# Optimization experiments

Measured on AMD Instinct MI355X. Metric: run time of the kernel, lower is better.

Reference implementation:

```python
import jax, jax.numpy as jnp
import numpy as np

FEATURE_SIZE = 10 * 64 * 64  # 40960
HIDDEN1 = 512
HIDDEN2 = 256
BATCH = 4096


def setup_inputs() -> dict:
    key = jax.random.key(0)
    ks = jax.random.split(key, 8)
    # Sparse binary-ish features emulated as dense uniform (math is identical).
    white_features = jax.random.uniform(ks[0], (BATCH, FEATURE_SIZE), dtype=jnp.float32)
    black_features = jax.random.uniform(ks[1], (BATCH, FEATURE_SIZE), dtype=jnp.float32)
    s_ft = 1.0 / np.sqrt(FEATURE_SIZE)
    s_fc1 = 1.0 / np.sqrt(HIDDEN1 * 2)
    s_fc2 = 1.0 / np.sqrt(HIDDEN2)
    ft_w = jax.random.uniform(ks[2], (HIDDEN1, FEATURE_SIZE), minval=-s_ft, maxval=s_ft, dtype=jnp.float32)
    ft_b = jax.random.uniform(ks[3], (HIDDEN1,), minval=-s_ft, maxval=s_ft, dtype=jnp.float32)
    fc1_w = jax.random.uniform(ks[4], (HIDDEN2, HIDDEN1 * 2), minval=-s_fc1, maxval=s_fc1, dtype=jnp.float32)
    fc1_b = jax.random.uniform(ks[5], (HIDDEN2,), minval=-s_fc1, maxval=s_fc1, dtype=jnp.float32)
    fc2_w = jax.random.uniform(ks[6], (1, HIDDEN2), minval=-s_fc2, maxval=s_fc2, dtype=jnp.float32)
    fc2_b = jax.random.uniform(ks[7], (1,), minval=-s_fc2, maxval=s_fc2, dtype=jnp.float32)
    return dict(white_features=white_features, black_features=black_features,
                ft_w=ft_w, ft_b=ft_b, fc1_w=fc1_w, fc1_b=fc1_b, fc2_w=fc2_w, fc2_b=fc2_b)


def reference(white_features, black_features, ft_w, ft_b, fc1_w, fc1_b, fc2_w, fc2_b):
    # Feature transform per perspective, clamped to [0, 1]
    white_ft = jnp.clip(white_features @ ft_w.T + ft_b, 0.0, 1.0)  # [B, H1]
    black_ft = jnp.clip(black_features @ ft_w.T + ft_b, 0.0, 1.0)  # [B, H1]
    combined = jnp.concatenate([white_ft, black_ft], axis=1)       # [B, 2*H1]
    x = jax.nn.relu(combined @ fc1_w.T + fc1_b)                    # [B, H2]
    x = x @ fc2_w.T + fc2_b                                        # [B, 1]
    return x.squeeze(-1)
```

## Files before the change

kernel.cpp:

```cpp
#include <hip/hip_runtime.h>
#include <stdint.h>

#define BATCH 4096
#define FEAT  40960
#define H1    512
#define KS    4
#define KCHUNK (FEAT / KS)
#define NSTEPS (KCHUNK / 32)
#define NTILES (FEAT / 32)
#define WTILE  32768
#define BUFSTRIDE 36864
#define ALDS 32768

typedef float f32x4 __attribute__((ext_vector_type(4)));
typedef short s16x8 __attribute__((ext_vector_type(8)));
typedef unsigned int u32x2 __attribute__((ext_vector_type(2)));
typedef unsigned int u32x4 __attribute__((ext_vector_type(4)));

__device__ __forceinline__ unsigned bfpack2(float lo, float hi) {
  unsigned a = __float_as_uint(lo);
  unsigned b = __float_as_uint(hi);
  a += 0x7FFFu + ((a >> 16) & 1u);
  b += 0x7FFFu + ((b >> 16) & 1u);
  return (a >> 16) | (b & 0xFFFF0000u);
}

__device__ __forceinline__ int lds_swz(int r, int cb) {
  return (r << 6) + (cb ^ (((r >> 1) & 3) << 4));
}

__device__ __forceinline__ void glds16(const void* g, void* l) {
  __builtin_amdgcn_global_load_lds(
      (const __attribute__((address_space(1))) unsigned*)g,
      (__attribute__((address_space(3))) unsigned*)l, 16, 0, 0);
}

__global__ __launch_bounds__(512)
void wcvt_kernel(const float* __restrict__ ftw, char* __restrict__ wbf) {
  const int bid = blockIdx.x;
  const int T = bid >> 2, rq = bid & 3;
  const int tid = threadIdx.x;
  const int r = rq * 128 + (tid >> 2), kq = tid & 3;
  const float* src = ftw + (size_t)r * FEAT + T * 32 + kq * 8;
  f32x4 v0 = *(const f32x4*)src;
  f32x4 v1 = *(const f32x4*)(src + 4);
  u32x4 o;
  o.x = bfpack2(v0.x, v0.y); o.y = bfpack2(v0.z, v0.w);
  o.z = bfpack2(v1.x, v1.y); o.w = bfpack2(v1.z, v1.w);
  *(u32x4*)(wbf + (size_t)T * WTILE + lds_swz(r, kq * 16)) = o;
}

__global__ __launch_bounds__(512, 4)
void ft_gemm_kernel(const float* __restrict__ whiteF,
                    const float* __restrict__ blackF,
                    const char* __restrict__ wbf,
                    float* __restrict__ Ppart) {
  __shared__ char smem[2 * BUFSTRIDE];

  const int tid = threadIdx.x, bid = blockIdx.x;
  const int wgid = (bid & 7) * 64 + (bid >> 3);
  const int ks = wgid >> 7;
  const int p  = (wgid >> 6) & 1;
  const int mt = wgid & 63;

  const float* Ag =
      (p == 0 ? whiteF : blackF) + (size_t)(mt * 64) * FEAT + ks * KCHUNK;

  const int a_row = tid >> 3, a_kq = tid & 7;
  const float* aptr = Ag + (size_t)a_row * FEAT + a_kq * 4;
  const int awoff = ALDS + lds_swz(a_row, a_kq * 8);

  const int lane = tid & 63, wave = tid >> 6;
  const char* wsrc = wbf + (size_t)ks * NSTEPS * WTILE + wave * 4096 + lane * 16;
  const int wdst = wave * 4096;

  const int wn = wave;
  const int lrow = lane & 15, lkb = (lane >> 4) * 16;
  int a_off[4], b_off[4];
#pragma unroll
  for (int m = 0; m < 4; ++m) a_off[m] = ALDS + lds_swz(m * 16 + lrow, lkb);
#pragma unroll
  for (int n = 0; n < 4; ++n) b_off[n] = lds_swz(wn * 64 + n * 16 + lrow, lkb);

  f32x4 acc[4][4];
#pragma unroll
  for (int m = 0; m < 4; ++m)
#pragma unroll
    for (int n = 0; n < 4; ++n) acc[m][n] = (f32x4){0.f, 0.f, 0.f, 0.f};

  f32x4 raA[2];

#pragma unroll
  for (int c = 0; c < 4; ++c) glds16(wsrc + c * 1024, smem + wdst + c * 1024);
  raA[0] = *(const f32x4*)aptr;

#define GSTEP(B, LAST, t)                                                     \
  {                                                                           \
    if (!(LAST)) raA[(B) ^ 1] = *(const f32x4*)(aptr + (size_t)((t) + 1) * 32); \
    u32x2 av;                                                                 \
    av.x = bfpack2(raA[B].x, raA[B].y);                                       \
    av.y = bfpack2(raA[B].z, raA[B].w);                                       \
    *(u32x2*)(smem + (B) * BUFSTRIDE + awoff) = av;                           \
    __builtin_amdgcn_sched_barrier(0);                                        \
    if (LAST) { asm volatile("s_waitcnt vmcnt(0) lgkmcnt(0)" ::: "memory"); } \
    else      { asm volatile("s_waitcnt vmcnt(1) lgkmcnt(0)" ::: "memory"); } \
    __builtin_amdgcn_sched_barrier(0);                                        \
    __builtin_amdgcn_s_barrier();                                             \
    __builtin_amdgcn_sched_barrier(0);                                        \
    const char* base = smem + (B) * BUFSTRIDE;                                \
    s16x8 af[4];                                                              \
    _Pragma("unroll") for (int m = 0; m < 4; ++m)                             \
        af[m] = *(const s16x8*)(base + a_off[m]);                             \
    if (!(LAST)) {                                                            \
      const char* wsp = wsrc + (size_t)((t) + 1) * WTILE;                     \
      char* wdp = smem + ((B) ^ 1) * BUFSTRIDE + wdst;                        \
      _Pragma("unroll") for (int c = 0; c < 4; ++c)                           \
          glds16(wsp + c * 1024, wdp + c * 1024);                             \
    }                                                                         \
    _Pragma("unroll") for (int n = 0; n < 4; ++n) {                           \
      s16x8 bfn = *(const s16x8*)(base + b_off[n]);                           \
      _Pragma("unroll") for (int m = 0; m < 4; ++m)                           \
          acc[m][n] = __builtin_amdgcn_mfma_f32_16x16x32_bf16(                \
              af[m], bfn, acc[m][n], 0, 0, 0);                                \
    }                                                                         \
  }

  for (int tt = 0; tt < NSTEPS - 2; tt += 2) {
    GSTEP(0, false, tt);
    GSTEP(1, false, tt + 1);
  }
  GSTEP(0, false, NSTEPS - 2);
  GSTEP(1, true, NSTEPS - 1);
#undef GSTEP

  float* Pp = Ppart + ((size_t)(ks * 2 + p) * BATCH + mt * 64) * H1;
  const int r0 = (lane >> 4) * 4;
  const int c0 = wn * 64 + lrow;
#pragma unroll
  for (int m = 0; m < 4; ++m)
#pragma unroll
    for (int n = 0; n < 4; ++n) {
      float* dst = Pp + (size_t)(r0 + m * 16) * H1 + c0 + n * 16;
#pragma unroll
      for (int j = 0; j < 4; ++j) dst[(size_t)j * H1] = acc[m][n][j];
    }
}

__global__ __launch_bounds__(256)
void ft_reduce_kernel(const float* __restrict__ Ppart,
                      const float* __restrict__ ftb,
                      unsigned short* __restrict__ comb) {
  const size_t gid = (size_t)blockIdx.x * 256 + threadIdx.x;
  const int    pp  = (int)(gid / (BATCH * H1 / 4));
  const size_t rem = gid % (BATCH * H1 / 4);
  const int    row = (int)(rem / (H1 / 4));
  const int    n4  = (int)(rem % (H1 / 4)) * 4;

  f32x4 s = (f32x4){0.f, 0.f, 0.f, 0.f};
#pragma unroll
  for (int ks = 0; ks < KS; ++ks)
    s += *(const f32x4*)(Ppart + ((size_t)(ks * 2 + pp) * BATCH + row) * H1 + n4);
  const f32x4 bv = *(const f32x4*)(ftb + n4);
  s += bv;
  s.x = fminf(fmaxf(s.x, 0.f), 1.f);
  s.y = fminf(fmaxf(s.y, 0.f), 1.f);
  s.z = fminf(fmaxf(s.z, 0.f), 1.f);
  s.w = fminf(fmaxf(s.w, 0.f), 1.f);

  u32x2 o;
  o.x = bfpack2(s.x, s.y);
  o.y = bfpack2(s.z, s.w);
  *(u32x2*)(comb + (size_t)row * 1024 + pp * H1 + n4) = o;
}

__global__ __launch_bounds__(256)
void fc_kernel(const unsigned short* __restrict__ comb,
               const float* __restrict__ w1, const float* __restrict__ b1,
               const float* __restrict__ w2, const float* __restrict__ b2,
               float* __restrict__ out) {
  __shared__ char smem[40960];
  __shared__ float rowsum[64];

  const int tid = threadIdx.x;
  const int bm  = blockIdx.x;
  if (tid < 64) rowsum[tid] = 0.f;

  const int a_row = tid >> 2, a_kq = tid & 3;
  const unsigned short* aptr = comb + (size_t)(bm * 64 + a_row) * 1024 + a_kq * 8;
  const float* wptr = w1 + (size_t)a_row * 1024 + a_kq * 8;

  u32x4 raA;
  f32x4 rw0[4], rw1[4];
  auto issue = [&](int t) {
    raA = *(const u32x4*)(aptr + t * 32);
    const float* wp = wptr + t * 32;
#pragma unroll
    for (int s = 0; s < 4; ++s) {
      rw0[s] = *(const f32x4*)(wp + (size_t)s * 64 * 1024);
      rw1[s] = *(const f32x4*)(wp + (size_t)s * 64 * 1024 + 4);
    }
  };

  const int aoff_w = lds_swz(a_row, a_kq * 16);
  int woff_w[4];
#pragma unroll
  for (int s = 0; s < 4; ++s)
    woff_w[s] = 4096 + lds_swz(s * 64 + a_row, a_kq * 16);

  auto cvtwrite = [&](int b) {
    char* base = smem + b * 20480;
    *(u32x4*)(base + aoff_w) = raA;
#pragma unroll
    for (int s = 0; s < 4; ++s) {
      u32x4 wv;
      wv.x = bfpack2(rw0[s].x, rw0[s].y); wv.y = bfpack2(rw0[s].z, rw0[s].w);
      wv.z = bfpack2(rw1[s].x, rw1[s].y); wv.w = bfpack2(rw1[s].z, rw1[s].w);
      *(u32x4*)(base + woff_w[s]) = wv;
    }
  };

  const int lane = tid & 63, wn = tid >> 6;
  const int lrow = lane & 15, lkb = (lane >> 4) * 16;
  int a_off[4], b_off[4];
#pragma unroll
  for (int m = 0; m < 4; ++m) a_off[m] = lds_swz(m * 16 + lrow, lkb);
#pragma unroll
  for (int n = 0; n < 4; ++n) b_off[n] = 4096 + lds_swz(wn * 64 + n * 16 + lrow, lkb);

  f32x4 acc[4][4];
#pragma unroll
  for (int m = 0; m < 4; ++m)
#pragma unroll
    for (int n = 0; n < 4; ++n) acc[m][n] = (f32x4){0.f, 0.f, 0.f, 0.f};

  issue(0);
  for (int t = 0; t < 32; ++t) {
    const int b = t & 1;
    cvtwrite(b);
    if (t + 1 < 32) issue(t + 1);
    asm volatile("s_waitcnt lgkmcnt(0)" ::: "memory");
    __builtin_amdgcn_sched_barrier(0);
    __builtin_amdgcn_s_barrier();
    __builtin_amdgcn_sched_barrier(0);
    char* base = smem + b * 20480;
    s16x8 af[4];
#pragma unroll
    for (int m = 0; m < 4; ++m) af[m] = *(const s16x8*)(base + a_off[m]);
#pragma unroll
    for (int n = 0; n < 4; ++n) {
      s16x8 bfn = *(const s16x8*)(base + b_off[n]);
#pragma unroll
      for (int m = 0; m < 4; ++m)
        acc[m][n] = __builtin_amdgcn_mfma_f32_16x16x32_bf16(af[m], bfn, acc[m][n], 0, 0, 0);
    }
  }

  float b1v[4], w2v[4];
#pragma unroll
  for (int n = 0; n < 4; ++n) {
    const int col = wn * 64 + n * 16 + lrow;
    b1v[n] = b1[col];
    w2v[n] = w2[col];
  }
#pragma unroll
  for (int m = 0; m < 4; ++m)
#pragma unroll
    for (int j = 0; j < 4; ++j) {
      float v = 0.f;
#pragma unroll
      for (int n = 0; n < 4; ++n) {
        float x = acc[m][n][j] + b1v[n];
        x = fmaxf(x, 0.f);
        v += x * w2v[n];
      }
#pragma unroll
      for (int d = 1; d < 16; d <<= 1) v += __shfl_xor(v, d, 64);
      if ((lane & 15) == 0)
        atomicAdd(&rowsum[m * 16 + (lane >> 4) * 4 + j], v);
    }
  __syncthreads();
  if (tid < 64) {
    out[bm * 64 + tid] = rowsum[tid] + b2[0];
  }
}

extern "C" void kernel_launch(void* const* d_in, const int* in_sizes, int n_in,
                              void* d_out, int out_size, void* d_ws, size_t ws_size,
                              hipStream_t stream) {
  const float* whiteF = (const float*)d_in[0];
  const float* blackF = (const float*)d_in[1];
  const float* ftw    = (const float*)d_in[2];
  const float* ftb    = (const float*)d_in[3];
  const float* w1     = (const float*)d_in[4];
  const float* b1     = (const float*)d_in[5];
  const float* w2     = (const float*)d_in[6];
  const float* b2     = (const float*)d_in[7];

  char* wbf = (char*)d_ws;
  const size_t wbf_bytes   = (size_t)NTILES * WTILE;
  const size_t ppart_bytes = (size_t)KS * 2 * BATCH * H1 * sizeof(float);
  float* Ppart = (float*)((char*)d_ws + wbf_bytes);
  unsigned short* comb = (unsigned short*)((char*)d_ws + wbf_bytes + ppart_bytes);
  float* outp = (float*)d_out;

  hipLaunchKernelGGL(wcvt_kernel, dim3(NTILES * 4), dim3(512), 0, stream, ftw, wbf);
  hipLaunchKernelGGL(ft_gemm_kernel, dim3(512), dim3(512), 0, stream,
                     whiteF, blackF, wbf, Ppart);
  hipLaunchKernelGGL(ft_reduce_kernel, dim3((2 * BATCH * H1 / 4) / 256), dim3(256),
                     0, stream, Ppart, ftb, comb);
  hipLaunchKernelGGL(fc_kernel, dim3(BATCH / 64), dim3(256), 0, stream,
                     comb, w1, b1, w2, b2, outp);
}
```

Baseline: 548.8 us.

## Load A fragments directly into registers and drop the workgroup barrier

The activation tile no longer goes through LDS. Each wave now loads its own MFMA A fragments straight from global memory, converts them with the hardware v_cvt_pk_bf16_f32 instruction, and prefetches the next step's fragments into registers. Because each wave only reads the weight region it copies into LDS itself, the per-step s_barrier is removed and the LDS footprint shrinks to two 32 KB weight buffers. The trade-off is that the A tile is read eight times per workgroup, once per wave, from global/cache, which adds cache traffic and register pressure.

```diff
diff --git a/kernel.cpp b/kernel.cpp
--- a/kernel.cpp
+++ b/kernel.cpp
@@ -9,8 +9,6 @@
 #define NSTEPS (KCHUNK / 32)
 #define NTILES (FEAT / 32)
 #define WTILE  32768
-#define BUFSTRIDE 36864
-#define ALDS 32768
 
 typedef float f32x4 __attribute__((ext_vector_type(4)));
 typedef short s16x8 __attribute__((ext_vector_type(8)));
@@ -23,6 +21,12 @@
   a += 0x7FFFu + ((a >> 16) & 1u);
   b += 0x7FFFu + ((b >> 16) & 1u);
   return (a >> 16) | (b & 0xFFFF0000u);
+}
+
+__device__ __forceinline__ unsigned cvtpk(float lo, float hi) {
+  unsigned r;
+  asm("v_cvt_pk_bf16_f32 %0, %1, %2" : "=v"(r) : "v"(lo), "v"(hi));
+  return r;
 }
 
 __device__ __forceinline__ int lds_swz(int r, int cb) {
@@ -55,7 +59,7 @@
                     const float* __restrict__ blackF,
                     const char* __restrict__ wbf,
                     float* __restrict__ Ppart) {
-  __shared__ char smem[2 * BUFSTRIDE];
+  __shared__ char smem[65536];
 
   const int tid = threadIdx.x, bid = blockIdx.x;
   const int wgid = (bid & 7) * 64 + (bid >> 3);
@@ -66,19 +70,19 @@
   const float* Ag =
       (p == 0 ? whiteF : blackF) + (size_t)(mt * 64) * FEAT + ks * KCHUNK;
 
-  const int a_row = tid >> 3, a_kq = tid & 7;
-  const float* aptr = Ag + (size_t)a_row * FEAT + a_kq * 4;
-  const int awoff = ALDS + lds_swz(a_row, a_kq * 8);
-
   const int lane = tid & 63, wave = tid >> 6;
+  const int lrow = lane & 15, lkb = (lane >> 4) * 16;
+
+  const float* am[4];
+#pragma unroll
+  for (int m = 0; m < 4; ++m)
+    am[m] = Ag + (size_t)(m * 16 + lrow) * FEAT + (lane >> 4) * 8;
+
   const char* wsrc = wbf + (size_t)ks * NSTEPS * WTILE + wave * 4096 + lane * 16;
   const int wdst = wave * 4096;
 
   const int wn = wave;
-  const int lrow = lane & 15, lkb = (lane >> 4) * 16;
-  int a_off[4], b_off[4];
-#pragma unroll
-  for (int m = 0; m < 4; ++m) a_off[m] = ALDS + lds_swz(m * 16 + lrow, lkb);
+  int b_off[4];
 #pragma unroll
   for (int n = 0; n < 4; ++n) b_off[n] = lds_swz(wn * 64 + n * 16 + lrow, lkb);
 
@@ -88,35 +92,47 @@
 #pragma unroll
     for (int n = 0; n < 4; ++n) acc[m][n] = (f32x4){0.f, 0.f, 0.f, 0.f};
 
-  f32x4 raA[2];
+  f32x4 raf[4][2];
 
 #pragma unroll
   for (int c = 0; c < 4; ++c) glds16(wsrc + c * 1024, smem + wdst + c * 1024);
-  raA[0] = *(const f32x4*)aptr;
+#pragma unroll
+  for (int m = 0; m < 4; ++m) {
+    raf[m][0] = *(const f32x4*)am[m];
+    raf[m][1] = *(const f32x4*)(am[m] + 4);
+  }
 
 #define GSTEP(B, LAST, t)                                                     \
   {                                                                           \
-    if (!(LAST)) raA[(B) ^ 1] = *(const f32x4*)(aptr + (size_t)((t) + 1) * 32); \
-    u32x2 av;                                                                 \
-    av.x = bfpack2(raA[B].x, raA[B].y);                                       \
-    av.y = bfpack2(raA[B].z, raA[B].w);                                       \
-    *(u32x2*)(smem + (B) * BUFSTRIDE + awoff) = av;                           \
+    asm volatile("s_waitcnt lgkmcnt(0)" ::: "memory");  \
     __builtin_amdgcn_sched_barrier(0);                                        \
-    if (LAST) { asm volatile("s_waitcnt vmcnt(0) lgkmcnt(0)" ::: "memory"); } \
-    else      { asm volatile("s_waitcnt vmcnt(1) lgkmcnt(0)" ::: "memory"); } \
-    __builtin_amdgcn_sched_barrier(0);                                        \
-    __builtin_amdgcn_s_barrier();                                             \
-    __builtin_amdgcn_sched_barrier(0);                                        \
-    const char* base = smem + (B) * BUFSTRIDE;                                \
-    s16x8 af[4];                                                              \
-    _Pragma("unroll") for (int m = 0; m < 4; ++m)                             \
-        af[m] = *(const s16x8*)(base + a_off[m]);                             \
     if (!(LAST)) {                                                            \
       const char* wsp = wsrc + (size_t)((t) + 1) * WTILE;                     \
-      char* wdp = smem + ((B) ^ 1) * BUFSTRIDE + wdst;                        \
+      char* wdp = smem + ((B) ^ 1) * 32768 + wdst;                            \
       _Pragma("unroll") for (int c = 0; c < 4; ++c)                           \
           glds16(wsp + c * 1024, wdp + c * 1024);                             \
     }                                                                         \
+    __builtin_amdgcn_sched_barrier(0);                                        \
+    if (LAST) { asm volatile("s_waitcnt vmcnt(0)" ::: "memory"); }            \
+    else      { asm volatile("s_waitcnt vmcnt(4)" ::: "memory"); }            \
+    __builtin_amdgcn_sched_barrier(0);                                        \
+    s16x8 af[4];                                                              \
+    _Pragma("unroll") for (int m = 0; m < 4; ++m) {                           \
+      u32x4 cv;                                                               \
+      cv.x = cvtpk(raf[m][0].x, raf[m][0].y);                                 \
+      cv.y = cvtpk(raf[m][0].z, raf[m][0].w);                                 \
+      cv.z = cvtpk(raf[m][1].x, raf[m][1].y);                                 \
+      cv.w = cvtpk(raf[m][1].z, raf[m][1].w);                                 \
+      af[m] = __builtin_bit_cast(s16x8, cv);                                  \
+    }                                                                         \
+    if (!(LAST)) {                                                            \
+      _Pragma("unroll") for (int m = 0; m < 4; ++m) {                         \
+        const float* ap = am[m] + (size_t)((t) + 1) * 32;                     \
+        raf[m][0] = *(const f32x4*)ap;                                        \
+        raf[m][1] = *(const f32x4*)(ap + 4);                                  \
+      }                                                                       \
+    }                                                                         \
+    const char* base = smem + (B) * 32768;                                    \
     _Pragma("unroll") for (int n = 0; n < 4; ++n) {                           \
       s16x8 bfn = *(const s16x8*)(base + b_off[n]);                           \
       _Pragma("unroll") for (int m = 0; m < 4; ++m)                           \
```

Result: slower. 1.462 ms (+166.5%).

## Load B fragments directly from pre-swizzled global into registers, skip LDS staging

Applied to the files above, without the earlier changes.

The weight-conversion kernel now writes bf16 weights in MFMA fragment order, so each lane's B operand is one contiguous 16-byte chunk. The GEMM loads B fragments straight from global memory into double-buffered registers instead of staging them through LDS. LDS is cut to a small double buffer for the A tile. This removes the B-tile LDS traffic and frees shared memory, at the cost of more VGPRs and exposing global-load latency that the old pipeline hid behind barriers.

```diff
diff --git a/kernel.cpp b/kernel.cpp
--- a/kernel.cpp
+++ b/kernel.cpp
@@ -9,8 +9,6 @@
 #define NSTEPS (KCHUNK / 32)
 #define NTILES (FEAT / 32)
 #define WTILE  32768
-#define BUFSTRIDE 36864
-#define ALDS 32768
 
 typedef float f32x4 __attribute__((ext_vector_type(4)));
 typedef short s16x8 __attribute__((ext_vector_type(8)));
@@ -29,25 +27,25 @@
   return (r << 6) + (cb ^ (((r >> 1) & 3) << 4));
 }
 
-__device__ __forceinline__ void glds16(const void* g, void* l) {
-  __builtin_amdgcn_global_load_lds(
-      (const __attribute__((address_space(1))) unsigned*)g,
-      (__attribute__((address_space(3))) unsigned*)l, 16, 0, 0);
-}
-
 __global__ __launch_bounds__(512)
 void wcvt_kernel(const float* __restrict__ ftw, char* __restrict__ wbf) {
-  const int bid = blockIdx.x;
-  const int T = bid >> 2, rq = bid & 3;
+  const int T = blockIdx.x;
   const int tid = threadIdx.x;
-  const int r = rq * 128 + (tid >> 2), kq = tid & 3;
-  const float* src = ftw + (size_t)r * FEAT + T * 32 + kq * 8;
-  f32x4 v0 = *(const f32x4*)src;
-  f32x4 v1 = *(const f32x4*)(src + 4);
-  u32x4 o;
-  o.x = bfpack2(v0.x, v0.y); o.y = bfpack2(v0.z, v0.w);
-  o.z = bfpack2(v1.x, v1.y); o.w = bfpack2(v1.z, v1.w);
-  *(u32x4*)(wbf + (size_t)T * WTILE + lds_swz(r, kq * 16)) = o;
+  const int c  = tid & 7;
+  const int r0 = tid >> 3;
+#pragma unroll
+  for (int pass = 0; pass < 8; ++pass) {
+    const int r = pass * 64 + r0;
+    const float* src = ftw + (size_t)r * FEAT + T * 32 + c * 4;
+    f32x4 v = *(const f32x4*)src;
+    u32x2 o;
+    o.x = bfpack2(v.x, v.y);
+    o.y = bfpack2(v.z, v.w);
+    const int nb = r >> 6, f = (r >> 4) & 3, lr = r & 15;
+    const int l = (c >> 1) * 16 + lr;
+    *(u32x2*)(wbf + (size_t)T * WTILE + ((nb * 4 + f) << 10) + l * 16 +
+              (c & 1) * 8) = o;
+  }
 }
 
 __global__ __launch_bounds__(512, 4)
@@ -55,7 +53,7 @@
                     const float* __restrict__ blackF,
                     const char* __restrict__ wbf,
                     float* __restrict__ Ppart) {
-  __shared__ char smem[2 * BUFSTRIDE];
+  __shared__ char smem[8192];
 
   const int tid = threadIdx.x, bid = blockIdx.x;
   const int wgid = (bid & 7) * 64 + (bid >> 3);
@@ -66,21 +64,19 @@
   const float* Ag =
       (p == 0 ? whiteF : blackF) + (size_t)(mt * 64) * FEAT + ks * KCHUNK;
 
-  const int a_row = tid >> 3, a_kq = tid & 7;
-  const float* aptr = Ag + (size_t)a_row * FEAT + a_kq * 4;
-  const int awoff = ALDS + lds_swz(a_row, a_kq * 8);
+  const int a_row = tid >> 3, a_kc = tid & 7;
+  const float* aptr = Ag + (size_t)a_row * FEAT + a_kc * 4;
+  const int awoff = lds_swz(a_row, a_kc * 8);
 
   const int lane = tid & 63, wave = tid >> 6;
-  const char* wsrc = wbf + (size_t)ks * NSTEPS * WTILE + wave * 4096 + lane * 16;
-  const int wdst = wave * 4096;
-
-  const int wn = wave;
   const int lrow = lane & 15, lkb = (lane >> 4) * 16;
-  int a_off[4], b_off[4];
-#pragma unroll
-  for (int m = 0; m < 4; ++m) a_off[m] = ALDS + lds_swz(m * 16 + lrow, lkb);
-#pragma unroll
-  for (int n = 0; n < 4; ++n) b_off[n] = lds_swz(wn * 64 + n * 16 + lrow, lkb);
+
+  const char* wsrc =
+      wbf + (size_t)ks * NSTEPS * WTILE + (wave << 12) + lane * 16;
+
+  int a_off[4];
+#pragma unroll
+  for (int m = 0; m < 4; ++m) a_off[m] = lds_swz(m * 16 + lrow, lkb);
 
   f32x4 acc[4][4];
 #pragma unroll
@@ -88,37 +84,38 @@
 #pragma unroll
     for (int n = 0; n < 4; ++n) acc[m][n] = (f32x4){0.f, 0.f, 0.f, 0.f};
 
-  f32x4 raA[2];
-
-#pragma unroll
-  for (int c = 0; c < 4; ++c) glds16(wsrc + c * 1024, smem + wdst + c * 1024);
-  raA[0] = *(const f32x4*)aptr;
+  f32x4 raA;
+  u32x4 rb[2][4];
+
+  raA = *(const f32x4*)aptr;
+#pragma unroll
+  for (int n = 0; n < 4; ++n)
+    rb[0][n] = *(const u32x4*)(wsrc + (n << 10));
 
 #define GSTEP(B, LAST, t)                                                     \
   {                                                                           \
-    if (!(LAST)) raA[(B) ^ 1] = *(const f32x4*)(aptr + (size_t)((t) + 1) * 32); \
+                    \
     u32x2 av;                                                                 \
-    av.x = bfpack2(raA[B].x, raA[B].y);                                       \
-    av.y = bfpack2(raA[B].z, raA[B].w);                                       \
-    *(u32x2*)(smem + (B) * BUFSTRIDE + awoff) = av;                           \
-    __builtin_amdgcn_sched_barrier(0);                                        \
-    if (LAST) { asm volatile("s_waitcnt vmcnt(0) lgkmcnt(0)" ::: "memory"); } \
-    else      { asm volatile("s_waitcnt vmcnt(1) lgkmcnt(0)" ::: "memory"); } \
+    av.x = bfpack2(raA.x, raA.y);                                             \
+    av.y = bfpack2(raA.z, raA.w);                                             \
+    *(u32x2*)(smem + (B) * 4096 + awoff) = av;                                \
+    if (!(LAST)) {    \
+      raA = *(const f32x4*)(aptr + (size_t)((t) + 1) * 32);                   \
+                                             \
+      const char* wsp = wsrc + (size_t)((t) + 1) * WTILE;                     \
+      _Pragma("unroll") for (int n = 0; n < 4; ++n)                           \
+          rb[(B) ^ 1][n] = *(const u32x4*)(wsp + (n << 10));                  \
+    }                                                                         \
+    asm volatile("s_waitcnt lgkmcnt(0)" ::: "memory");   \
     __builtin_amdgcn_sched_barrier(0);                                        \
     __builtin_amdgcn_s_barrier();                                             \
     __builtin_amdgcn_sched_barrier(0);                                        \
-    const char* base = smem + (B) * BUFSTRIDE;                                \
+    const char* base = smem + (B) * 4096;                                     \
     s16x8 af[4];                                                              \
     _Pragma("unroll") for (int m = 0; m < 4; ++m)                             \
         af[m] = *(const s16x8*)(base + a_off[m]);                             \
-    if (!(LAST)) {                                                            \
-      const char* wsp = wsrc + (size_t)((t) + 1) * WTILE;                     \
-      char* wdp = smem + ((B) ^ 1) * BUFSTRIDE + wdst;                        \
-      _Pragma("unroll") for (int c = 0; c < 4; ++c)                           \
-          glds16(wsp + c * 1024, wdp + c * 1024);                             \
-    }                                                                         \
     _Pragma("unroll") for (int n = 0; n < 4; ++n) {                           \
-      s16x8 bfn = *(const s16x8*)(base + b_off[n]);                           \
+      s16x8 bfn = __builtin_bit_cast(s16x8, rb[B][n]);                        \
       _Pragma("unroll") for (int m = 0; m < 4; ++m)                           \
           acc[m][n] = __builtin_amdgcn_mfma_f32_16x16x32_bf16(                \
               af[m], bfn, acc[m][n], 0, 0, 0);                                \
@@ -135,7 +132,7 @@
 
   float* Pp = Ppart + ((size_t)(ks * 2 + p) * BATCH + mt * 64) * H1;
   const int r0 = (lane >> 4) * 4;
-  const int c0 = wn * 64 + lrow;
+  const int c0 = wave * 64 + lrow;
 #pragma unroll
   for (int m = 0; m < 4; ++m)
 #pragma unroll
@@ -303,7 +300,7 @@
   unsigned short* comb = (unsigned short*)((char*)d_ws + wbf_bytes + ppart_bytes);
   float* outp = (float*)d_out;
 
-  hipLaunchKernelGGL(wcvt_kernel, dim3(NTILES * 4), dim3(512), 0, stream, ftw, wbf);
+  hipLaunchKernelGGL(wcvt_kernel, dim3(NTILES), dim3(512), 0, stream, ftw, wbf);
   hipLaunchKernelGGL(ft_gemm_kernel, dim3(512), dim3(512), 0, stream,
                      whiteF, blackF, wbf, Ppart);
   hipLaunchKernelGGL(ft_reduce_kernel, dim3((2 * BATCH * H1 / 4) / 256), dim3(256),
```

Result: no change. 553.6 us (+0.9%).

## Enlarge FT GEMM tile to 256x256 with K=64 steps and phased MFMA pipeline

Applied to the files above, without the earlier changes.

Restructures the feature-transform GEMM so each workgroup computes a 256-row by 256-column tile with 64-wide K steps. Each workgroup now covers half of H1 instead of all of it, and the weight image is repacked into an MFMA-fragment-friendly layout. The main loop is split into barrier-separated phases with setprio around MFMA bursts, and activations are prefetched two steps ahead in registers. The aim is more data reuse per LDS byte and less A-matrix global traffic per FLOP, at the cost of 128KB LDS, higher register pressure, lower occupancy and only 256 workgroups.

```diff
diff --git a/kernel.cpp b/kernel.cpp
--- a/kernel.cpp
+++ b/kernel.cpp
@@ -6,11 +6,10 @@
 #define H1    512
 #define KS    4
 #define KCHUNK (FEAT / KS)
-#define NSTEPS (KCHUNK / 32)
-#define NTILES (FEAT / 32)
-#define WTILE  32768
-#define BUFSTRIDE 36864
-#define ALDS 32768
+#define NT    (KCHUNK / 64)
+#define NT64  (FEAT / 64)
+#define WIMG  65536
+#define ABOFF 65536
 
 typedef float f32x4 __attribute__((ext_vector_type(4)));
 typedef short s16x8 __attribute__((ext_vector_type(8)));
@@ -35,109 +34,201 @@
       (__attribute__((address_space(3))) unsigned*)l, 16, 0, 0);
 }
 
+#define PHASE_BAR()                    \
+  do {                                 \
+    __builtin_amdgcn_sched_barrier(0); \
+    __builtin_amdgcn_s_barrier();      \
+    __builtin_amdgcn_sched_barrier(0); \
+  } while (0)
+
 __global__ __launch_bounds__(512)
 void wcvt_kernel(const float* __restrict__ ftw, char* __restrict__ wbf) {
-  const int bid = blockIdx.x;
-  const int T = bid >> 2, rq = bid & 3;
+  const int T = blockIdx.x;
   const int tid = threadIdx.x;
-  const int r = rq * 128 + (tid >> 2), kq = tid & 3;
-  const float* src = ftw + (size_t)r * FEAT + T * 32 + kq * 8;
-  f32x4 v0 = *(const f32x4*)src;
-  f32x4 v1 = *(const f32x4*)(src + 4);
-  u32x4 o;
-  o.x = bfpack2(v0.x, v0.y); o.y = bfpack2(v0.z, v0.w);
-  o.z = bfpack2(v1.x, v1.y); o.w = bfpack2(v1.z, v1.w);
-  *(u32x4*)(wbf + (size_t)T * WTILE + lds_swz(r, kq * 16)) = o;
-}
-
-__global__ __launch_bounds__(512, 4)
+  const int c = tid & 7;
+  const int r0 = tid >> 3;
+#pragma unroll
+  for (int pass = 0; pass < 8; ++pass) {
+    const int r = pass * 64 + r0;
+    const float* src = ftw + (size_t)r * FEAT + T * 64 + c * 8;
+    f32x4 v0 = *(const f32x4*)src;
+    f32x4 v1 = *(const f32x4*)(src + 4);
+    u32x4 o;
+    o.x = bfpack2(v0.x, v0.y); o.y = bfpack2(v0.z, v0.w);
+    o.z = bfpack2(v1.x, v1.y); o.w = bfpack2(v1.z, v1.w);
+    const int lane = (c & 3) * 16 + (r & 15);
+    *(u32x4*)(wbf + (size_t)T * WIMG + (r >> 8) * 32768 +
+              ((r >> 4) & 15) * 2048 + (c >> 2) * 1024 + lane * 16) = o;
+  }
+}
+
+__global__ __launch_bounds__(512, 2)
 void ft_gemm_kernel(const float* __restrict__ whiteF,
                     const float* __restrict__ blackF,
                     const char* __restrict__ wbf,
                     float* __restrict__ Ppart) {
-  __shared__ char smem[2 * BUFSTRIDE];
+  __shared__ char smem[131072];
 
   const int tid = threadIdx.x, bid = blockIdx.x;
-  const int wgid = (bid & 7) * 64 + (bid >> 3);
-  const int ks = wgid >> 7;
-  const int p  = (wgid >> 6) & 1;
-  const int mt = wgid & 63;
+  const int nt = bid & 1;
+  const int ks = (bid >> 1) & 3;
+  const int p  = (bid >> 3) & 1;
+  const int mt = bid >> 4;
 
   const float* Ag =
-      (p == 0 ? whiteF : blackF) + (size_t)(mt * 64) * FEAT + ks * KCHUNK;
-
-  const int a_row = tid >> 3, a_kq = tid & 7;
-  const float* aptr = Ag + (size_t)a_row * FEAT + a_kq * 4;
-  const int awoff = ALDS + lds_swz(a_row, a_kq * 8);
+      (p == 0 ? whiteF : blackF) + (size_t)(mt * 256) * FEAT + ks * KCHUNK;
 
   const int lane = tid & 63, wave = tid >> 6;
-  const char* wsrc = wbf + (size_t)ks * NSTEPS * WTILE + wave * 4096 + lane * 16;
-  const int wdst = wave * 4096;
-
-  const int wn = wave;
-  const int lrow = lane & 15, lkb = (lane >> 4) * 16;
-  int a_off[4], b_off[4];
-#pragma unroll
-  for (int m = 0; m < 4; ++m) a_off[m] = ALDS + lds_swz(m * 16 + lrow, lkb);
-#pragma unroll
-  for (int n = 0; n < 4; ++n) b_off[n] = lds_swz(wn * 64 + n * 16 + lrow, lkb);
-
-  f32x4 acc[4][4];
-#pragma unroll
-  for (int m = 0; m < 4; ++m)
+  const int wm = wave >> 2, wn = wave & 3;
+  const int lrow = lane & 15, lkq = lane >> 4;
+  const int rx7 = lrow & 7;
+
+  const int ar = tid >> 1, ah = tid & 1;
+  const float* aptr = Ag + (size_t)ar * FEAT + ah * 32;
+  int awr[4];
+#pragma unroll
+  for (int i = 0; i < 4; ++i)
+    awr[i] = ar * 128 + (((ah * 4 + i) ^ (ar & 7)) << 4);
+
+  int ard[8];
+#pragma unroll
+  for (int m = 0; m < 8; ++m) ard[m] = (wm * 128 + m * 16 + lrow) * 128;
+  const int co0 = (lkq ^ rx7) << 4;
+
+  const char* wimg = wbf + (size_t)(ks * NT) * WIMG + nt * 32768;
+  int wrd[4];
+#pragma unroll
+  for (int n = 0; n < 4; ++n) wrd[n] = (wn * 4 + n) * 2048 + lane * 16;
+  const int ws0 = (wave * 2) * 2048 + lane * 16;
+
+  f32x4 acc[8][4];
+#pragma unroll
+  for (int m = 0; m < 8; ++m)
 #pragma unroll
     for (int n = 0; n < 4; ++n) acc[m][n] = (f32x4){0.f, 0.f, 0.f, 0.f};
 
-  f32x4 raA[2];
-
-#pragma unroll
-  for (int c = 0; c < 4; ++c) glds16(wsrc + c * 1024, smem + wdst + c * 1024);
-  raA[0] = *(const f32x4*)aptr;
-
-#define GSTEP(B, LAST, t)                                                     \
+  f32x4 rA[8];
+
+#pragma unroll
+  for (int i = 0; i < 8; ++i) rA[i] = *(const f32x4*)(aptr + i * 4);
+#pragma unroll
+  for (int q = 0; q < 2; ++q)
+#pragma unroll
+    for (int j = 0; j < 2; ++j)
+      glds16(wimg + ws0 + q * 2048 + j * 1024,
+             smem + ws0 + q * 2048 + j * 1024 - lane * 16 + lane * 16);
+  {
+#pragma unroll
+    for (int i = 0; i < 4; ++i) {
+      u32x4 o;
+      o.x = bfpack2(rA[2 * i].x, rA[2 * i].y);
+      o.y = bfpack2(rA[2 * i].z, rA[2 * i].w);
+      o.z = bfpack2(rA[2 * i + 1].x, rA[2 * i + 1].y);
+      o.w = bfpack2(rA[2 * i + 1].z, rA[2 * i + 1].w);
+      *(u32x4*)(smem + ABOFF + awr[i]) = o;
+    }
+  }
+#pragma unroll
+  for (int i = 0; i < 8; ++i) rA[i] = *(const f32x4*)(aptr + 64 + i * 4);
+  asm volatile("s_waitcnt lgkmcnt(0)" ::: "memory");
+  PHASE_BAR();
+
+#define GSTEP(B, t)                                                           \
   {                                                                           \
-    if (!(LAST)) raA[(B) ^ 1] = *(const f32x4*)(aptr + (size_t)((t) + 1) * 32); \
-    u32x2 av;                                                                 \
-    av.x = bfpack2(raA[B].x, raA[B].y);                                       \
-    av.y = bfpack2(raA[B].z, raA[B].w);                                       \
-    *(u32x2*)(smem + (B) * BUFSTRIDE + awoff) = av;                           \
+    const char* Wb = smem + (B) * 32768;                                      \
+    const char* Ab = smem + ABOFF + (B) * 32768;                              \
+            \
+    asm volatile("s_waitcnt vmcnt(8)" ::: "memory");                          \
+    PHASE_BAR();                                                              \
+    s16x8 af[4], wf[4];                                                       \
+    _Pragma("unroll") for (int m = 0; m < 4; ++m)                             \
+        af[m] = *(const s16x8*)(Ab + ard[m] + co0);                           \
+    _Pragma("unroll") for (int n = 0; n < 4; ++n)                             \
+        wf[n] = *(const s16x8*)(Wb + wrd[n]);                                 \
+    {                                                                         \
+      const int t1 = ((t) + 1 < NT) ? (t) + 1 : NT - 1;                       \
+      const char* ws = wimg + (size_t)t1 * WIMG + ws0;                        \
+      char* wd = smem + ((B) ^ 1) * 32768 + ws0 - 0;                          \
+      _Pragma("unroll") for (int q = 0; q < 2; ++q)                           \
+        _Pragma("unroll") for (int j = 0; j < 2; ++j)                         \
+            glds16(ws + q * 2048 + j * 1024, wd + q * 2048 + j * 1024);       \
+    }                                                                         \
+    asm volatile("s_waitcnt lgkmcnt(0)" ::: "memory");                        \
     __builtin_amdgcn_sched_barrier(0);                                        \
-    if (LAST) { asm volatile("s_waitcnt vmcnt(0) lgkmcnt(0)" ::: "memory"); } \
-    else      { asm volatile("s_waitcnt vmcnt(1) lgkmcnt(0)" ::: "memory"); } \
-    __builtin_amdgcn_sched_barrier(0);                                        \
-    __builtin_amdgcn_s_barrier();                                             \
-    __builtin_amdgcn_sched_barrier(0);                                        \
-    const char* base = smem + (B) * BUFSTRIDE;                                \
-    s16x8 af[4];                                                              \
-    _Pragma("unroll") for (int m = 0; m < 4; ++m)                             \
-        af[m] = *(const s16x8*)(base + a_off[m]);                             \
-    if (!(LAST)) {                                                            \
-      const char* wsp = wsrc + (size_t)((t) + 1) * WTILE;                     \
-      char* wdp = smem + ((B) ^ 1) * BUFSTRIDE + wdst;                        \
-      _Pragma("unroll") for (int c = 0; c < 4; ++c)                           \
-          glds16(wsp + c * 1024, wdp + c * 1024);                             \
-    }                                                                         \
-    _Pragma("unroll") for (int n = 0; n < 4; ++n) {                           \
-      s16x8 bfn = *(const s16x8*)(base + b_off[n]);                           \
+    __builtin_amdgcn_s_setprio(1);                                            \
+    _Pragma("unroll") for (int n = 0; n < 4; ++n)                             \
       _Pragma("unroll") for (int m = 0; m < 4; ++m)                           \
           acc[m][n] = __builtin_amdgcn_mfma_f32_16x16x32_bf16(                \
-              af[m], bfn, acc[m][n], 0, 0, 0);                                \
+              af[m], wf[n], acc[m][n], 0, 0, 0);                              \
+    __builtin_amdgcn_s_setprio(0);                                            \
+                                    \
+    PHASE_BAR();                                                              \
+    s16x8 ag[4];                                                              \
+    _Pragma("unroll") for (int m = 0; m < 4; ++m)                             \
+        ag[m] = *(const s16x8*)(Ab + ard[4 + m] + co0);                       \
+    asm volatile("s_waitcnt lgkmcnt(0)" ::: "memory");                        \
+    __builtin_amdgcn_sched_barrier(0);                                        \
+    __builtin_amdgcn_s_setprio(1);                                            \
+    _Pragma("unroll") for (int n = 0; n < 4; ++n)                             \
+      _Pragma("unroll") for (int m = 0; m < 4; ++m)                           \
+          acc[4 + m][n] = __builtin_amdgcn_mfma_f32_16x16x32_bf16(            \
+              ag[m], wf[n], acc[4 + m][n], 0, 0, 0);                          \
+    __builtin_amdgcn_s_setprio(0);                                            \
+           \
+    PHASE_BAR();                                                              \
+    _Pragma("unroll") for (int i = 0; i < 4; ++i) {                           \
+      u32x4 o;                                                                \
+      o.x = bfpack2(rA[2 * i].x, rA[2 * i].y);                                \
+      o.y = bfpack2(rA[2 * i].z, rA[2 * i].w);                                \
+      o.z = bfpack2(rA[2 * i + 1].x, rA[2 * i + 1].y);                        \
+      o.w = bfpack2(rA[2 * i + 1].z, rA[2 * i + 1].w);                        \
+      *(u32x4*)(smem + ABOFF + ((B) ^ 1) * 32768 + awr[i]) = o;               \
     }                                                                         \
-  }
-
-  for (int tt = 0; tt < NSTEPS - 2; tt += 2) {
-    GSTEP(0, false, tt);
-    GSTEP(1, false, tt + 1);
-  }
-  GSTEP(0, false, NSTEPS - 2);
-  GSTEP(1, true, NSTEPS - 1);
+    {                                                                         \
+      const int t2 = ((t) + 2 < NT) ? (t) + 2 : NT - 1;                       \
+      _Pragma("unroll") for (int i = 0; i < 8; ++i)                           \
+          rA[i] = *(const f32x4*)(aptr + (size_t)t2 * 64 + i * 4);            \
+    }                                                                         \
+    _Pragma("unroll") for (int n = 0; n < 4; ++n)                             \
+        wf[n] = *(const s16x8*)(Wb + wrd[n] + 1024);                          \
+    _Pragma("unroll") for (int m = 0; m < 4; ++m)                             \
+        af[m] = *(const s16x8*)(Ab + ard[m] + (co0 ^ 64));                    \
+    asm volatile("s_waitcnt lgkmcnt(0)" ::: "memory");                        \
+    __builtin_amdgcn_sched_barrier(0);                                        \
+    __builtin_amdgcn_s_setprio(1);                                            \
+    _Pragma("unroll") for (int n = 0; n < 4; ++n)                             \
+      _Pragma("unroll") for (int m = 0; m < 4; ++m)                           \
+          acc[m][n] = __builtin_amdgcn_mfma_f32_16x16x32_bf16(                \
+              af[m], wf[n], acc[m][n], 0, 0, 0);                              \
+    __builtin_amdgcn_s_setprio(0);                                            \
+                                                        \
+    PHASE_BAR();                                                              \
+    _Pragma("unroll") for (int m = 0; m < 4; ++m)                             \
+        ag[m] = *(const s16x8*)(Ab + ard[4 + m] + (co0 ^ 64));                \
+    asm volatile("s_waitcnt lgkmcnt(0)" ::: "memory");                        \
+    __builtin_amdgcn_sched_barrier(0);                                        \
+    __builtin_amdgcn_s_setprio(1);                                            \
+    _Pragma("unroll") for (int n = 0; n < 4; ++n)                             \
+      _Pragma("unroll") for (int m = 0; m < 4; ++m)                           \
+          acc[4 + m][n] = __builtin_amdgcn_mfma_f32_16x16x32_bf16(            \
+              ag[m], wf[n], acc[4 + m][n], 0, 0, 0);                          \
+    __builtin_amdgcn_s_setprio(0);                                            \
+  }
+
+  for (int tt = 0; tt < NT; tt += 2) {
+    GSTEP(0, tt);
+    GSTEP(1, tt + 1);
+  }
 #undef GSTEP
 
-  float* Pp = Ppart + ((size_t)(ks * 2 + p) * BATCH + mt * 64) * H1;
-  const int r0 = (lane >> 4) * 4;
-  const int c0 = wn * 64 + lrow;
-#pragma unroll
-  for (int m = 0; m < 4; ++m)
+  asm volatile("s_waitcnt vmcnt(0) lgkmcnt(0)" ::: "memory");
+  __builtin_amdgcn_sched_barrier(0);
+
+  float* Pp = Ppart + ((size_t)(ks * 2 + p) * BATCH + mt * 256) * H1;
+  const int r0 = wm * 128 + lkq * 4;
+  const int c0 = nt * 256 + wn * 64 + lrow;
+#pragma unroll
+  for (int m = 0; m < 8; ++m)
 #pragma unroll
     for (int n = 0; n < 4; ++n) {
       float* dst = Pp + (size_t)(r0 + m * 16) * H1 + c0 + n * 16;
@@ -297,14 +388,14 @@
   const float* b2     = (const float*)d_in[7];
 
   char* wbf = (char*)d_ws;
-  const size_t wbf_bytes   = (size_t)NTILES * WTILE;
+  const size_t wbf_bytes   = (size_t)NT64 * WIMG;
   const size_t ppart_bytes = (size_t)KS * 2 * BATCH * H1 * sizeof(float);
   float* Ppart = (float*)((char*)d_ws + wbf_bytes);
   unsigned short* comb = (unsigned short*)((char*)d_ws + wbf_bytes + ppart_bytes);
   float* outp = (float*)d_out;
 
-  hipLaunchKernelGGL(wcvt_kernel, dim3(NTILES * 4), dim3(512), 0, stream, ftw, wbf);
-  hipLaunchKernelGGL(ft_gemm_kernel, dim3(512), dim3(512), 0, stream,
+  hipLaunchKernelGGL(wcvt_kernel, dim3(NT64), dim3(512), 0, stream, ftw, wbf);
+  hipLaunchKernelGGL(ft_gemm_kernel, dim3(256), dim3(512), 0, stream,
                      whiteF, blackF, wbf, Ppart);
   hipLaunchKernelGGL(ft_reduce_kernel, dim3((2 * BATCH * H1 / 4) / 256), dim3(256),
                      0, stream, Ppart, ftb, comb);
```

New measurement: 1.052 ms. +91.7%, slower.
